# Optimization experiments

Measured on AMD Instinct MI355X. Metric: run time of the kernel, lower is better.

Reference implementation:

```python
import jax, jax.numpy as jnp
import numpy as np

B, T, E, H, V = 64, 32, 300, 1024, 10000


def setup_inputs() -> dict:
    key = jax.random.key(0)
    ks = jax.random.split(key, 12)
    s = lambda fan: 1.0 / np.sqrt(fan)
    return {
        "questions": jax.random.randint(ks[0], (B, T), 0, V, dtype=jnp.int64) if jax.config.jax_enable_x64 else jax.random.randint(ks[0], (B, T), 0, V, dtype=jnp.int32),
        "question_lengths": jax.random.randint(ks[1], (B,), 1, T + 1, dtype=jnp.int32),
        "embed_table": jax.random.normal(ks[2], (V, E), jnp.float32) * 0.02,
        "W_ih1": jax.random.normal(ks[3], (4 * H, E), jnp.float32) * s(H),
        "W_hh1": jax.random.normal(ks[4], (4 * H, H), jnp.float32) * s(H),
        "b_ih1": jax.random.normal(ks[5], (4 * H,), jnp.float32) * s(H),
        "b_hh1": jax.random.normal(ks[6], (4 * H,), jnp.float32) * s(H),
        "W_ih2": jax.random.normal(ks[7], (4 * H, H), jnp.float32) * s(H),
        "W_hh2": jax.random.normal(ks[8], (4 * H, H), jnp.float32) * s(H),
        "b_ih2": jax.random.normal(ks[9], (4 * H,), jnp.float32) * s(H),
        "b_hh2": jax.random.normal(ks[10], (4 * H,), jnp.float32) * s(H),
    }


def _lstm_cell(x_t, h, c, W_ih, W_hh, b_ih, b_hh):
    # PyTorch LSTMCell: gate order i, f, g, o
    gates = x_t @ W_ih.T + b_ih + h @ W_hh.T + b_hh  # [B, 4H]
    i, f, g, o = jnp.split(gates, 4, axis=-1)
    c_new = jax.nn.sigmoid(f) * c + jax.nn.sigmoid(i) * jnp.tanh(g)
    h_new = jax.nn.sigmoid(o) * jnp.tanh(c_new)
    return h_new, c_new


def reference(questions, question_lengths, embed_table,
              W_ih1, W_hh1, b_ih1, b_hh1, W_ih2, W_hh2, b_ih2, b_hh2):
    x = embed_table[questions]                      # [B, T, E]
    b, t, _ = x.shape
    h = W_hh1.shape[1]

    def step(carry, inp):
        h1, c1, h2, c2 = carry
        x_t, m = inp                                # x_t [B,E], m [B,1] bool
        h1n, c1n = _lstm_cell(x_t, h1, c1, W_ih1, W_hh1, b_ih1, b_hh1)
        h2n, c2n = _lstm_cell(h1n, h2, c2, W_ih2, W_hh2, b_ih2, b_hh2)
        # samples past their length keep their final state frozen
        h1 = jnp.where(m, h1n, h1); c1 = jnp.where(m, c1n, c1)
        h2 = jnp.where(m, h2n, h2); c2 = jnp.where(m, c2n, c2)
        return (h1, c1, h2, c2), None

    mask = jnp.arange(t)[None, :] < question_lengths[:, None]      # [B,T]
    xs = (jnp.swapaxes(x, 0, 1), jnp.swapaxes(mask, 0, 1)[..., None])
    init = tuple(jnp.zeros((b, h), x.dtype) for _ in range(4))
    (h1, c1, h2, c2), _ = jax.lax.scan(step, init, xs)

    # tile final top-layer hidden to [B, H, 28, 28]
    E_q = jnp.broadcast_to(h2[:, None, None, :], (b, 28, 28, h))
    E_q = jnp.transpose(E_q, (0, 3, 2, 1))
    return (E_q, h1[:, None, :], h2[:, None, :], c1[:, None, :], c2[:, None, :])
```

## Files before the change

### kernel.cpp

```cpp
#include <hip/hip_runtime.h>
#include <hip/hip_bf16.h>
#include <cstdint>

#define B_  64
#define T_  32
#define E_  300
#define EP  320
#define H_  1024
#define G4  4096
#define BH  65536
#define NBLK 192

typedef __attribute__((ext_vector_type(8))) short bf16x8;
typedef __attribute__((ext_vector_type(4))) float f32x4;
typedef unsigned short ushort_t;

__device__ __forceinline__ bf16x8 load_b8(const ushort_t* p) {
    union { uint4 u; bf16x8 v; } c;
    c.u = *reinterpret_cast<const uint4*>(p);
    return c.v;
}

__device__ __forceinline__ ushort_t f2bf(float x) {
    union { float f; uint32_t u; } c; c.f = x;
    uint32_t r = c.u + 0x7fffu + ((c.u >> 16) & 1u);
    return (ushort_t)(r >> 16);
}

__device__ __forceinline__ float sigm(float x) { return 1.0f / (1.0f + __expf(-x)); }

__device__ __forceinline__ void astore64(uint64_t* p, uint64_t v) {
    __hip_atomic_store(p, v, __ATOMIC_RELAXED, __HIP_MEMORY_SCOPE_AGENT);
}
__device__ __forceinline__ uint64_t packf2(float a, float b) {
    union { float f[2]; uint64_t u; } c; c.f[0] = a; c.f[1] = b; return c.u;
}

__device__ __forceinline__ void setflag(int* flags, int role, int js, int val) {
    __hip_atomic_store(&flags[(role * 64 + js) * 16], val,
                       __ATOMIC_RELAXED, __HIP_MEMORY_SCOPE_AGENT);
}
__device__ __forceinline__ void waitwave(const int* flags, int role, int target, int lane) {
    const int* p = &flags[(role * 64 + lane) * 16];
    int guard = 0;
    for (;;) {
        int v = __hip_atomic_load(p, __ATOMIC_RELAXED, __HIP_MEMORY_SCOPE_AGENT);
        if (__all(v >= target)) return;
        if (++guard > (1 << 22)) return;
        __builtin_amdgcn_s_sleep(1);
    }
}

__global__ void prep_inputs(const int* __restrict__ q, const float* __restrict__ table,
                            ushort_t* __restrict__ Xp,
                            const float* __restrict__ Wsrc, ushort_t* __restrict__ Wdst) {
    int blk = blockIdx.x;
    if (blk < 1280) {
        int i = blk * 256 + threadIdx.x;
        const int n = B_ * T_ * EP;
        for (; i < n; i += 1280 * 256) {
            int r = i / EP, c = i - r * EP;
            Xp[i] = (c < E_) ? f2bf(table[q[r] * E_ + c]) : (ushort_t)0;
        }
    } else {
        int i = (blk - 1280) * 256 + threadIdx.x;
        const int n = G4 * EP;
        for (; i < n; i += 2048 * 256) {
            int r = i / EP, c = i - r * EP;
            Wdst[i] = (c < E_) ? f2bf(Wsrc[r * E_ + c]) : (ushort_t)0;
        }
    }
}

__launch_bounds__(256)
__global__ void xgemm(const ushort_t* __restrict__ Xp, const ushort_t* __restrict__ Wp,
                      const float* __restrict__ b_ih1, const float* __restrict__ b_hh1,
                      float* __restrict__ xg) {
    int mblk = blockIdx.x, nblk = blockIdx.y;
    int wave = threadIdx.x >> 6, lane = threadIdx.x & 63;
    int lm = lane & 15, lq = lane >> 4;
    int m0 = mblk * 64 + wave * 16;
    f32x4 acc[4];
    #pragma unroll
    for (int g = 0; g < 4; ++g) {
        int n = nblk * 64 + g * 16 + lm;
        float bv = b_ih1[n] + b_hh1[n];
        acc[g] = (f32x4){bv, bv, bv, bv};
    }
    for (int k0 = 0; k0 < EP; k0 += 32) {
        bf16x8 a = load_b8(Xp + (m0 + lm) * EP + k0 + lq * 8);
        #pragma unroll
        for (int g = 0; g < 4; ++g) {
            bf16x8 b = load_b8(Wp + (nblk * 64 + g * 16 + lm) * EP + k0 + lq * 8);
            acc[g] = __builtin_amdgcn_mfma_f32_16x16x32_bf16(a, b, acc[g], 0, 0, 0);
        }
    }
    #pragma unroll
    for (int g = 0; g < 4; ++g)
        #pragma unroll
        for (int r = 0; r < 4; ++r) {
            int m = m0 + lq * 4 + r;
            int b = m >> 5, t = m & 31;
            int n = nblk * 64 + g * 16 + lm;
            xg[((size_t)t * B_ + b) * G4 + n] = acc[g][r];
        }
}


__device__ __forceinline__ void gemm_k1024(const ushort_t* __restrict__ hvec,
                                           const ushort_t (*w)[1032],
                                           int lm, int lq, int m0, f32x4 acc[4]) {
    const uint4* hr = reinterpret_cast<const uint4*>(hvec + (size_t)(m0 + lm) * H_);
    uint4 buf[32];
    #pragma unroll
    for (int grp = 0; grp < 4; ++grp)
        #pragma unroll
        for (int i = 0; i < 8; ++i)
            buf[grp * 8 + i] = hr[grp * 32 + i * 4 + lq];
    #pragma unroll
    for (int grp = 0; grp < 4; ++grp)
        #pragma unroll
        for (int i = 0; i < 8; ++i) {
            int k0 = grp * 256 + i * 32;
            union { uint4 u; bf16x8 v; } a; a.u = buf[grp * 8 + i];
            #pragma unroll
            for (int g = 0; g < 4; ++g) {
                bf16x8 bb = load_b8(&w[g * 16 + lm][k0 + lq * 8]);
                acc[g] = __builtin_amdgcn_mfma_f32_16x16x32_bf16(a.v, bb, acc[g], 0, 0, 0);
            }
        }
}

__device__ __forceinline__ void lstm_elem(const f32x4 acc[4], int r,
                                          float* c, float* h, ushort_t* hb) {
    float iv = sigm(acc[0][r]);
    float fv = sigm(acc[1][r]);
    float gv = tanhf(acc[2][r]);
    float ov = sigm(acc[3][r]);
    float cn = fv * c[r] + iv * gv;
    float hv = ov * tanhf(cn);
    c[r] = cn; h[r] = hv; hb[r] = f2bf(hv);
}

__device__ __forceinline__ void store_h_tile(ushort_t* dst, int js, const ushort_t* hst) {
    int tid = threadIdx.x;
    uint64_t v = reinterpret_cast<const uint64_t*>(hst)[tid];
    astore64(reinterpret_cast<uint64_t*>(dst + (size_t)(tid >> 2) * H_ + js * 16) + (tid & 3), v);
}

__global__ __launch_bounds__(256) void lstm_persist(
    const float* __restrict__ Whh1, const float* __restrict__ Wih2,
    const float* __restrict__ Whh2,
    const float* __restrict__ b_ih2, const float* __restrict__ b_hh2,
    const float* __restrict__ xg, const int* __restrict__ qlen,
    ushort_t* __restrict__ h1hist,
    ushort_t* __restrict__ h2hist,
    float* __restrict__ Qhist,
    float* __restrict__ h1f, float* __restrict__ c1f,
    float* __restrict__ h2f, float* __restrict__ c2f,
    int* __restrict__ flags)
{
    __shared__ ushort_t ws[64][1032];
    __shared__ __align__(16) ushort_t hstage[64][16];

    const int blk  = blockIdx.x;
    const int role = blk >> 6;
    const int js   = blk & 63;
    const int wave = threadIdx.x >> 6, lane = threadIdx.x & 63;
    const int lm = lane & 15, lq = lane >> 4;
    const int m0 = wave * 16;

    const float* Wsrc = (role == 0) ? Whh1 : (role == 1) ? Wih2 : Whh2;
    for (int idx = threadIdx.x; idx < 64 * 256; idx += 256) {
        int r = idx >> 8, c4 = idx & 255;
        int grow = (r >> 4) * H_ + js * 16 + (r & 15);
        float4 v = reinterpret_cast<const float4*>(Wsrc + (size_t)grow * H_)[c4];
        uint2 pk;
        pk.x = (uint32_t)f2bf(v.x) | ((uint32_t)f2bf(v.y) << 16);
        pk.y = (uint32_t)f2bf(v.z) | ((uint32_t)f2bf(v.w) << 16);
        *reinterpret_cast<uint2*>(&ws[r][c4 * 4]) = pk;
    }
    __syncthreads();

    int q[4];
    #pragma unroll
    for (int r = 0; r < 4; ++r) q[r] = qlen[m0 + lq * 4 + r];

    float    c_reg[4]  = {0.f, 0.f, 0.f, 0.f};
    float    h_reg[4]  = {0.f, 0.f, 0.f, 0.f};
    ushort_t hb_reg[4] = {0, 0, 0, 0};

    if (role == 0) {
        for (int t = 0; t < T_; ++t) {
            f32x4 acc[4];
            #pragma unroll
            for (int g = 0; g < 4; ++g)
                #pragma unroll
                for (int r = 0; r < 4; ++r)
                    acc[g][r] = xg[((size_t)t * B_ + (m0 + lq * 4 + r)) * G4 + g * H_ + js * 16 + lm];
            if (t > 0) {
                if (wave == 0) waitwave(flags, 0, t, lane);
                __syncthreads();
            }
            gemm_k1024(h1hist + (size_t)t * BH, ws, lm, lq, m0, acc);
            #pragma unroll
            for (int r = 0; r < 4; ++r) {
                if (t < q[r]) lstm_elem(acc, r, c_reg, h_reg, hb_reg);
                hstage[m0 + lq * 4 + r][lm] = hb_reg[r];
            }
            __syncthreads();
            store_h_tile(h1hist + (size_t)(t + 1) * BH, js, &hstage[0][0]);
            __syncthreads();
            if (threadIdx.x == 0) setflag(flags, 0, js, t + 1);
        }
        #pragma unroll
        for (int r = 0; r < 4; ++r) {
            int b = m0 + lq * 4 + r, j = js * 16 + lm;
            h1f[b * H_ + j] = h_reg[r]; c1f[b * H_ + j] = c_reg[r];
        }
    } else if (role == 1) {
        float bi[4];
        #pragma unroll
        for (int g = 0; g < 4; ++g) {
            int n = g * H_ + js * 16 + lm;
            bi[g] = b_ih2[n] + b_hh2[n];
        }
        for (int t = 0; t < T_; ++t) {
            if (wave == 0) waitwave(flags, 0, t + 1, lane);
            __syncthreads();
            f32x4 acc[4];
            #pragma unroll
            for (int g = 0; g < 4; ++g) acc[g] = (f32x4){bi[g], bi[g], bi[g], bi[g]};
            gemm_k1024(h1hist + (size_t)(t + 1) * BH, ws, lm, lq, m0, acc);
            uint64_t* Qw64 = (uint64_t*)(Qhist + (size_t)t * (4 * BH));
            #pragma unroll
            for (int r = 0; r < 4; ++r) {
                int b = m0 + lq * 4 + r, j = js * 16 + lm;
                size_t base = ((size_t)b * H_ + j) * 2;
                astore64(Qw64 + base,     packf2(acc[0][r], acc[1][r]));
                astore64(Qw64 + base + 1, packf2(acc[2][r], acc[3][r]));
            }
            __syncthreads();
            if (threadIdx.x == 0) setflag(flags, 1, js, t + 1);
        }
    } else {
        for (int t = 0; t < T_; ++t) {
            if (t > 0) {
                if (wave == 0)      waitwave(flags, 1, t + 1, lane);
                else if (wave == 1) waitwave(flags, 2, t,     lane);
            } else {
                if (wave == 0)      waitwave(flags, 1, 1,     lane);
            }
            __syncthreads();
            const uint4* Qr = (const uint4*)(Qhist + (size_t)t * (4 * BH));
            uint4 qp[4];
            #pragma unroll
            for (int r = 0; r < 4; ++r)
                qp[r] = Qr[(size_t)(m0 + lq * 4 + r) * H_ + js * 16 + lm];
            f32x4 acc[4];
            #pragma unroll
            for (int g = 0; g < 4; ++g) acc[g] = (f32x4){0.f, 0.f, 0.f, 0.f};
            gemm_k1024(h2hist + (size_t)t * BH, ws, lm, lq, m0, acc);
            #pragma unroll
            for (int r = 0; r < 4; ++r) {
                union { uint32_t u; float f; } x0, x1, x2, x3;
                x0.u = qp[r].x; x1.u = qp[r].y; x2.u = qp[r].z; x3.u = qp[r].w;
                acc[0][r] += x0.f; acc[1][r] += x1.f;
                acc[2][r] += x2.f; acc[3][r] += x3.f;
            }
            #pragma unroll
            for (int r = 0; r < 4; ++r) {
                if (t < q[r]) lstm_elem(acc, r, c_reg, h_reg, hb_reg);
                hstage[m0 + lq * 4 + r][lm] = hb_reg[r];
            }
            __syncthreads();
            store_h_tile(h2hist + (size_t)(t + 1) * BH, js, &hstage[0][0]);
            __syncthreads();
            if (t < T_ - 1 && threadIdx.x == 0) setflag(flags, 2, js, t + 1);
        }
        #pragma unroll
        for (int r = 0; r < 4; ++r) {
            int b = m0 + lq * 4 + r, j = js * 16 + lm;
            h2f[b * H_ + j] = h_reg[r]; c2f[b * H_ + j] = c_reg[r];
        }
    }
}

__global__ void write_out(const float* __restrict__ h1f, const float* __restrict__ h2f,
                          const float* __restrict__ c1f, const float* __restrict__ c2f,
                          float* __restrict__ out) {
    const long long EQ = (long long)B_ * H_ * 784;
    const long long n4 = (EQ + 4LL * B_ * H_) / 4;
    long long i4 = (long long)blockIdx.x * blockDim.x + threadIdx.x;
    long long stride = (long long)gridDim.x * blockDim.x;
    for (; i4 < n4; i4 += stride) {
        long long f = i4 * 4;
        float4 v;
        if (f < EQ) {
            long long bh = f / 784;
            float val = h2f[bh];
            v = make_float4(val, val, val, val);
        } else {
            long long r = f - EQ;
            int which = (int)(r >> 16);
            int j = (int)(r & 65535);
            const float* src = (which == 0) ? h1f : (which == 1) ? h2f : (which == 2) ? c1f : c2f;
            v = *reinterpret_cast<const float4*>(src + j);
        }
        reinterpret_cast<float4*>(out)[i4] = v;
    }
}

extern "C" void kernel_launch(void* const* d_in, const int* in_sizes, int n_in,
                              void* d_out, int out_size, void* d_ws, size_t ws_size,
                              hipStream_t stream) {
    const int*   questions = (const int*)d_in[0];
    const int*   qlen      = (const int*)d_in[1];
    const float* embed     = (const float*)d_in[2];
    const float* W_ih1     = (const float*)d_in[3];
    const float* W_hh1     = (const float*)d_in[4];
    const float* b_ih1     = (const float*)d_in[5];
    const float* b_hh1     = (const float*)d_in[6];
    const float* W_ih2     = (const float*)d_in[7];
    const float* W_hh2     = (const float*)d_in[8];
    const float* b_ih2     = (const float*)d_in[9];
    const float* b_hh2     = (const float*)d_in[10];
    float* out = (float*)d_out;

    char* w = (char*)d_ws;
    float*    xg     = (float*)(w + 0);
    ushort_t* Wih1p  = (ushort_t*)(w + 33554432);
    ushort_t* Xp     = (ushort_t*)(w + 36175872);
    int*      flags  = (int*)(w + 36175872);
    ushort_t* h1hist = (ushort_t*)(w + 37486592);
    ushort_t* h2hist = (ushort_t*)(w + 41811968);
    float*    Qhist  = (float*)(w + 46137344);
    float*    h1f    = (float*)(w + 79691776);
    float*    c1f    = (float*)(w + 79953920);
    float*    h2f    = (float*)(w + 80216064);
    float*    c2f    = (float*)(w + 80478208);

    hipMemsetAsync(w + 37486592, 0, 131072, stream);
    hipMemsetAsync(w + 41811968, 0, 131072, stream);

    prep_inputs<<<3328, 256, 0, stream>>>(questions, embed, Xp, W_ih1, Wih1p);
    xgemm<<<dim3(32, 64), 256, 0, stream>>>(Xp, Wih1p, b_ih1, b_hh1, xg);

    hipMemsetAsync(w + 36175872, 0, 12288, stream);

    lstm_persist<<<NBLK, 256, 0, stream>>>(W_hh1, W_ih2, W_hh2, b_ih2, b_hh2,
                                           xg, qlen,
                                           h1hist, h2hist, Qhist,
                                           h1f, c1f, h2f, c2f, flags);

    write_out<<<4096, 256, 0, stream>>>(h1f, h2f, c1f, c2f, out);
}
```

Baseline: 631.9 us.

## Use column-block h history layout, XOR-swizzled weight LDS, gate-interleaved xg

The hidden-state history is now stored in a column-block-major layout, so each block's 16-column tile store becomes one contiguous 2KB write and the GEMM reads h fragments from the new layout. The weight slice in shared memory drops the padding and uses an XOR swizzle to avoid bank conflicts. The input-gate precompute buffer is interleaved by gate, so layer-1 blocks load all four gates with a single 16-byte load per row instead of scattered scalar loads. The aim is to cut global memory transactions on the serial recurrence critical path. The cost is more complex indexing, which must stay consistent across producers and consumers.

```diff
diff --git a/kernel.cpp b/kernel.cpp
--- a/kernel.cpp
+++ b/kernel.cpp
@@ -102,21 +102,24 @@
             int m = m0 + lq * 4 + r;
             int b = m >> 5, t = m & 31;
             int n = nblk * 64 + g * 16 + lm;
-            xg[((size_t)t * B_ + b) * G4 + n] = acc[g][r];
-        }
-}
-
-
-__device__ __forceinline__ void gemm_k1024(const ushort_t* __restrict__ hvec,
-                                           const ushort_t (*w)[1032],
-                                           int lm, int lq, int m0, f32x4 acc[4]) {
-    const uint4* hr = reinterpret_cast<const uint4*>(hvec + (size_t)(m0 + lm) * H_);
+            int gate = n >> 10, j = n & 1023;
+            xg[(((size_t)t * B_ + b) * H_ + j) * 4 + gate] = acc[g][r];
+        }
+}
+
+
+__device__ __forceinline__ void gemm_cm(const ushort_t* __restrict__ hslot,
+                                        const ushort_t* __restrict__ wsf,
+                                        int lm, int lq, int m0, f32x4 acc[4]) {
+    const uint4* hr = reinterpret_cast<const uint4*>(hslot);
+    const int rbase = (m0 + lm) * 2 + (lq & 1);
+    const int cbo = lq >> 1;
     uint4 buf[32];
     #pragma unroll
     for (int grp = 0; grp < 4; ++grp)
         #pragma unroll
         for (int i = 0; i < 8; ++i)
-            buf[grp * 8 + i] = hr[grp * 32 + i * 4 + lq];
+            buf[grp * 8 + i] = hr[(grp * 16 + i * 2 + cbo) * 128 + rbase];
     #pragma unroll
     for (int grp = 0; grp < 4; ++grp)
         #pragma unroll
@@ -125,7 +128,8 @@
             union { uint4 u; bf16x8 v; } a; a.u = buf[grp * 8 + i];
             #pragma unroll
             for (int g = 0; g < 4; ++g) {
-                bf16x8 bb = load_b8(&w[g * 16 + lm][k0 + lq * 8]);
+                int row = g * 16 + lm;
+                bf16x8 bb = load_b8(wsf + row * 1024 + ((k0 + lq * 8) ^ ((lm & 7) << 3)));
                 acc[g] = __builtin_amdgcn_mfma_f32_16x16x32_bf16(a.v, bb, acc[g], 0, 0, 0);
             }
         }
@@ -142,10 +146,10 @@
     c[r] = cn; h[r] = hv; hb[r] = f2bf(hv);
 }
 
-__device__ __forceinline__ void store_h_tile(ushort_t* dst, int js, const ushort_t* hst) {
+__device__ __forceinline__ void store_h_tile(ushort_t* slot, int js, const ushort_t* hst) {
     int tid = threadIdx.x;
     uint64_t v = reinterpret_cast<const uint64_t*>(hst)[tid];
-    astore64(reinterpret_cast<uint64_t*>(dst + (size_t)(tid >> 2) * H_ + js * 16) + (tid & 3), v);
+    astore64(reinterpret_cast<uint64_t*>(slot) + js * 256 + tid, v);
 }
 
 __global__ __launch_bounds__(256) void lstm_persist(
@@ -160,7 +164,7 @@
     float* __restrict__ h2f, float* __restrict__ c2f,
     int* __restrict__ flags)
 {
-    __shared__ ushort_t ws[64][1032];
+    __shared__ ushort_t ws[64 * 1024];
     __shared__ __align__(16) ushort_t hstage[64][16];
 
     const int blk  = blockIdx.x;
@@ -171,6 +175,7 @@
     const int m0 = wave * 16;
 
     const float* Wsrc = (role == 0) ? Whh1 : (role == 1) ? Wih2 : Whh2;
+    uint2* wsp = reinterpret_cast<uint2*>(ws);
     for (int idx = threadIdx.x; idx < 64 * 256; idx += 256) {
         int r = idx >> 8, c4 = idx & 255;
         int grow = (r >> 4) * H_ + js * 16 + (r & 15);
@@ -178,7 +183,7 @@
         uint2 pk;
         pk.x = (uint32_t)f2bf(v.x) | ((uint32_t)f2bf(v.y) << 16);
         pk.y = (uint32_t)f2bf(v.z) | ((uint32_t)f2bf(v.w) << 16);
-        *reinterpret_cast<uint2*>(&ws[r][c4 * 4]) = pk;
+        wsp[r * 256 + (c4 ^ ((r & 7) << 1))] = pk;
     }
     __syncthreads();
 
@@ -192,17 +197,24 @@
 
     if (role == 0) {
         for (int t = 0; t < T_; ++t) {
-            f32x4 acc[4];
-            #pragma unroll
-            for (int g = 0; g < 4; ++g)
-                #pragma unroll
-                for (int r = 0; r < 4; ++r)
-                    acc[g][r] = xg[((size_t)t * B_ + (m0 + lq * 4 + r)) * G4 + g * H_ + js * 16 + lm];
+            uint4 xq[4];
+            #pragma unroll
+            for (int r = 0; r < 4; ++r)
+                xq[r] = reinterpret_cast<const uint4*>(xg)
+                        [((size_t)t * B_ + (m0 + lq * 4 + r)) * H_ + js * 16 + lm];
             if (t > 0) {
                 if (wave == 0) waitwave(flags, 0, t, lane);
                 __syncthreads();
             }
-            gemm_k1024(h1hist + (size_t)t * BH, ws, lm, lq, m0, acc);
+            f32x4 acc[4];
+            #pragma unroll
+            for (int r = 0; r < 4; ++r) {
+                union { uint32_t u; float f; } x0, x1, x2, x3;
+                x0.u = xq[r].x; x1.u = xq[r].y; x2.u = xq[r].z; x3.u = xq[r].w;
+                acc[0][r] = x0.f; acc[1][r] = x1.f;
+                acc[2][r] = x2.f; acc[3][r] = x3.f;
+            }
+            gemm_cm(h1hist + (size_t)t * BH, ws, lm, lq, m0, acc);
             #pragma unroll
             for (int r = 0; r < 4; ++r) {
                 if (t < q[r]) lstm_elem(acc, r, c_reg, h_reg, hb_reg);
@@ -231,7 +243,7 @@
             f32x4 acc[4];
             #pragma unroll
             for (int g = 0; g < 4; ++g) acc[g] = (f32x4){bi[g], bi[g], bi[g], bi[g]};
-            gemm_k1024(h1hist + (size_t)(t + 1) * BH, ws, lm, lq, m0, acc);
+            gemm_cm(h1hist + (size_t)(t + 1) * BH, ws, lm, lq, m0, acc);
             uint64_t* Qw64 = (uint64_t*)(Qhist + (size_t)t * (4 * BH));
             #pragma unroll
             for (int r = 0; r < 4; ++r) {
@@ -260,7 +272,7 @@
             f32x4 acc[4];
             #pragma unroll
             for (int g = 0; g < 4; ++g) acc[g] = (f32x4){0.f, 0.f, 0.f, 0.f};
-            gemm_k1024(h2hist + (size_t)t * BH, ws, lm, lq, m0, acc);
+            gemm_cm(h2hist + (size_t)t * BH, ws, lm, lq, m0, acc);
             #pragma unroll
             for (int r = 0; r < 4; ++r) {
                 union { uint32_t u; float f; } x0, x1, x2, x3;
```

Result: faster. 619.2 us (-2.0%).
